# Performance work log

Measured on AMD Instinct MI355X. Metric: run time of the kernel, lower is better.

The kernel has to match this reference:

```python
import jax, jax.numpy as jnp
import numpy as np
from jax import lax

N, E, F, H, B = 16384, 262144, 32, 128, 16
DI, DS, DC, DTR = 256, 16, 4, 8   # Mamba: d_inner=expand*H, d_state, d_conv, dt_rank=ceil(H/16)
NS, NC = 512, 8                   # num_stations, num line colors
EPS = 1e-5


def _forward(node_features, edge_index, batch, W_in, b_in, W_g1, b_g1, W_g2, b_g2,
             W_inproj, conv_w, conv_b, W_xproj, W_dt, b_dt, A_log, D_p, W_out,
             gamma, beta, Wc, bc, Wh, bh, Wt, bt, Wp1, bp1, Wp2, bp2, Wd, bd, Ws, bs):
    def gcn(x, W, b):
        # GCNConv with self-loops and symmetric normalization
        loops = jnp.arange(N)
        s = jnp.concatenate([edge_index[0], loops])
        d = jnp.concatenate([edge_index[1], loops])
        deg = jax.ops.segment_sum(jnp.ones(s.shape[0], x.dtype), d, num_segments=N)
        dinv = jnp.where(deg > 0, lax.rsqrt(deg), 0.0)
        xw = x @ W
        msg = xw[s] * (dinv[s] * dinv[d])[:, None]
        return jax.ops.segment_sum(msg, d, num_segments=N) + b

    h = jax.nn.relu(node_features @ W_in + b_in)
    h = jax.nn.relu(gcn(h, W_g1, b_g1))
    h_gnn = jax.nn.relu(gcn(h, W_g2, b_g2))

    # --- Mamba block over the node sequence (batch dim of 1, seq_len = N) ---
    xz = h_gnn @ W_inproj                      # (N, 2*DI)
    x, z = xz[:, :DI], xz[:, DI:]
    xp = jnp.pad(x, ((DC - 1, 0), (0, 0)))     # causal depthwise conv1d
    xc = conv_b + sum(xp[k:k + N] * conv_w[:, k] for k in range(DC))
    x = jax.nn.silu(xc)
    dbl = x @ W_xproj                          # (N, DTR + 2*DS)
    dt = jax.nn.softplus(dbl[:, :DTR] @ W_dt + b_dt)   # (N, DI)
    Bm = dbl[:, DTR:DTR + DS]                  # (N, DS)
    Cm = dbl[:, DTR + DS:]                     # (N, DS)
    A = -jnp.exp(A_log)                        # (DI, DS)
    dA = jnp.exp(dt[:, :, None] * A[None])     # (N, DI, DS)
    dBx = dt[:, :, None] * Bm[:, None, :] * x[:, :, None]

    def step(hst, t):
        dA_t, dBx_t, C_t = t
        hst = dA_t * hst + dBx_t               # (DI, DS)
        return hst, hst @ C_t                  # (DI,)

    _, ys = lax.scan(step, jnp.zeros((DI, DS), x.dtype), (dA, dBx, Cm))
    y = (ys + D_p * x) * jax.nn.silu(z)
    h_mamba = y @ W_out                        # (N, H)

    # residual + LayerNorm
    hh = h_gnn + h_mamba
    mu = hh.mean(-1, keepdims=True)
    var = ((hh - mu) ** 2).mean(-1, keepdims=True)
    h_final = (hh - mu) * lax.rsqrt(var + EPS) * gamma + beta

    # global_mean_pool per graph
    counts = jax.ops.segment_sum(jnp.ones(N, h_final.dtype), batch, num_segments=B)
    ge = jax.ops.segment_sum(h_final, batch, num_segments=B) / jnp.maximum(counts, 1.0)[:, None]

    # critic + all policy heads, concatenated: [1,4,3,NS,NS,NS,NC]
    return jnp.concatenate([ge @ Wc + bc, ge @ Wh + bh, ge @ Wt + bt,
                            ge @ Wp1 + bp1, ge @ Wp2 + bp2, ge @ Wd + bd,
                            ge @ Ws + bs], axis=-1)


def setup_inputs() -> dict:
    key = jax.random.key(0)
    ks = list(jax.random.split(key, 20))
    p = lambda i, shape, s=0.02: jax.random.normal(ks[i], shape, jnp.float32) * s
    return dict(
        node_features=jax.random.normal(ks[0], (N, F), jnp.float32),
        edge_index=jax.random.randint(ks[1], (2, E), 0, N),
        batch=jnp.sort(jax.random.randint(ks[2], (N,), 0, B)),
        W_in=p(3, (F, H)), b_in=jnp.zeros((H,), jnp.float32),
        W_g1=p(4, (H, H)), b_g1=jnp.zeros((H,), jnp.float32),
        W_g2=p(5, (H, H)), b_g2=jnp.zeros((H,), jnp.float32),
        W_inproj=p(6, (H, 2 * DI)),
        conv_w=p(7, (DI, DC)), conv_b=jnp.zeros((DI,), jnp.float32),
        W_xproj=p(8, (DI, DTR + 2 * DS)),
        W_dt=p(9, (DTR, DI)), b_dt=jnp.full((DI,), -4.0, jnp.float32),
        A_log=jnp.log(jnp.broadcast_to(jnp.arange(1.0, DS + 1.0, dtype=jnp.float32), (DI, DS))),
        D_p=jnp.ones((DI,), jnp.float32),
        W_out=p(10, (DI, H)),
        gamma=jnp.ones((H,), jnp.float32), beta=jnp.zeros((H,), jnp.float32),
        Wc=p(11, (H, 1)), bc=jnp.zeros((1,), jnp.float32),
        Wh=p(12, (H, 4)), bh=jnp.zeros((4,), jnp.float32),
        Wt=p(13, (H, 3)), bt=jnp.zeros((3,), jnp.float32),
        Wp1=p(14, (H, NS)), bp1=jnp.zeros((NS,), jnp.float32),
        Wp2=p(15, (H, NS)), bp2=jnp.zeros((NS,), jnp.float32),
        Wd=p(16, (H, NS)), bd=jnp.zeros((NS,), jnp.float32),
        Ws=p(17, (H, NC)), bs=jnp.zeros((NC,), jnp.float32),
    )


def reference(node_features, edge_index, batch, W_in, b_in, W_g1, b_g1, W_g2, b_g2,
              W_inproj, conv_w, conv_b, W_xproj, W_dt, b_dt, A_log, D_p, W_out,
              gamma, beta, Wc, bc, Wh, bh, Wt, bt, Wp1, bp1, Wp2, bp2, Wd, bd, Ws, bs):
    return _forward(node_features, edge_index, batch, W_in, b_in, W_g1, b_g1, W_g2, b_g2,
                    W_inproj, conv_w, conv_b, W_xproj, W_dt, b_dt, A_log, D_p, W_out,
                    gamma, beta, Wc, bc, Wh, bh, Wt, bt, Wp1, bp1, Wp2, bp2, Wd, bd, Ws, bs)
```

## Files before the change

kernel.cpp:

```cpp
#include <hip/hip_runtime.h>
#include <math.h>

#define NN 16384
#define EE 262144
#define FF 32
#define HH 128
#define BB 16
#define DI 256
#define DS 16
#define DC 4
#define DTR 8
#define OUTW 1552
#define NCH 256
#define CHLEN 64
#define NG 8
#define GL 32

__device__ __forceinline__ float siluf(float v) { return v / (1.f + __expf(-v)); }
__device__ __forceinline__ float softplusf(float v) {
    return fmaxf(v, 0.f) + __logf(1.f + __expf(-fabsf(v)));
}

__global__ void deg_kernel(const int* __restrict__ dst, int* __restrict__ cnt) {
    int e = blockIdx.x * blockDim.x + threadIdx.x;
    if (e < EE) atomicAdd(&cnt[dst[e]], 1);
}

__global__ __launch_bounds__(1024) void prefix_kernel(const int* __restrict__ cnt,
                                                      int* __restrict__ rowptr,
                                                      int* __restrict__ cursor,
                                                      float* __restrict__ dinv) {
    __shared__ int part[1024];
    int tid = threadIdx.x;
    int4 c4[4];
#pragma unroll
    for (int j = 0; j < 4; j++) c4[j] = ((const int4*)cnt)[tid * 4 + j];
    int v[16] = {c4[0].x, c4[0].y, c4[0].z, c4[0].w, c4[1].x, c4[1].y, c4[1].z, c4[1].w,
                 c4[2].x, c4[2].y, c4[2].z, c4[2].w, c4[3].x, c4[3].y, c4[3].z, c4[3].w};
    int s = 0;
#pragma unroll
    for (int j = 0; j < 16; j++) s += v[j];
    part[tid] = s;
    __syncthreads();
    for (int off = 1; off < 1024; off <<= 1) {
        int t = (tid >= off) ? part[tid - off] : 0;
        __syncthreads();
        part[tid] += t;
        __syncthreads();
    }
    int running = part[tid] - s;
    int rp[16];
    float dv[16];
#pragma unroll
    for (int j = 0; j < 16; j++) {
        rp[j] = running;
        running += v[j];
        dv[j] = rsqrtf((float)(v[j] + 1));
    }
#pragma unroll
    for (int j = 0; j < 4; j++) {
        int4 r4; r4.x = rp[j*4]; r4.y = rp[j*4+1]; r4.z = rp[j*4+2]; r4.w = rp[j*4+3];
        ((int4*)rowptr)[tid * 4 + j] = r4;
        ((int4*)cursor)[tid * 4 + j] = r4;
        float4 d4; d4.x = dv[j*4]; d4.y = dv[j*4+1]; d4.z = dv[j*4+2]; d4.w = dv[j*4+3];
        ((float4*)dinv)[tid * 4 + j] = d4;
    }
    if (tid == 1023) rowptr[NN] = part[1023];
}

__global__ void scatter_kernel(const int* __restrict__ src, const int* __restrict__ dst,
                               int* __restrict__ cursor, int* __restrict__ col) {
    int e = blockIdx.x * blockDim.x + threadIdx.x;
    if (e < EE) {
        int d = dst[e];
        int pos = atomicAdd(&cursor[d], 1);
        col[pos] = src[e];
    }
}

__global__ __launch_bounds__(256) void gemm_k(const float* __restrict__ A,
                                              const float* __restrict__ B,
                                              const float* __restrict__ bias,
                                              float* __restrict__ C,
                                              int M, int Nn, int K, int act) {
    __shared__ float As[16][68];
    __shared__ float Bs[16][68];
    int tid = threadIdx.x;
    int m0 = blockIdx.y * 64;
    int n0 = blockIdx.x * 64;
    int ty = tid >> 4, tx = tid & 15;
    float acc[4][4] = {{0.f}};
    for (int k0 = 0; k0 < K; k0 += 16) {
#pragma unroll
        for (int l = 0; l < 4; l++) {
            int idx = tid + l * 256;
            int i = idx >> 4, j = idx & 15;
            As[j][i] = A[(size_t)(m0 + i) * K + k0 + j];
        }
#pragma unroll
        for (int l = 0; l < 4; l++) {
            int idx = tid + l * 256;
            int i = idx >> 6, j = idx & 63;
            int n = n0 + j;
            Bs[i][j] = (n < Nn) ? B[(size_t)(k0 + i) * Nn + n] : 0.f;
        }
        __syncthreads();
#pragma unroll
        for (int kk = 0; kk < 16; kk++) {
            float4 a4 = *(const float4*)&As[kk][ty * 4];
            float4 b4 = *(const float4*)&Bs[kk][tx * 4];
            float av[4] = {a4.x, a4.y, a4.z, a4.w};
            float bv[4] = {b4.x, b4.y, b4.z, b4.w};
#pragma unroll
            for (int r = 0; r < 4; r++)
#pragma unroll
                for (int c = 0; c < 4; c++) acc[r][c] = fmaf(av[r], bv[c], acc[r][c]);
        }
        __syncthreads();
    }
    int nb = n0 + tx * 4;
    if (nb < Nn) {
        float4 bi4 = {0.f, 0.f, 0.f, 0.f};
        if (bias) bi4 = *(const float4*)&bias[nb];
#pragma unroll
        for (int r = 0; r < 4; r++) {
            int m = m0 + ty * 4 + r;
            float4 v;
            v.x = acc[r][0] + bi4.x; v.y = acc[r][1] + bi4.y;
            v.z = acc[r][2] + bi4.z; v.w = acc[r][3] + bi4.w;
            if (act == 1) {
                v.x = fmaxf(v.x, 0.f); v.y = fmaxf(v.y, 0.f);
                v.z = fmaxf(v.z, 0.f); v.w = fmaxf(v.w, 0.f);
            }
            *(float4*)&C[(size_t)m * Nn + nb] = v;
        }
    }
}

__global__ __launch_bounds__(256, 4) void gemm_big(const float* __restrict__ A,
                                                   const float* __restrict__ B,
                                                   float* __restrict__ C,
                                                   int M, int Nn, int K) {
    __shared__ float As[16][132];
    __shared__ float Bs[16][132];
    int tid = threadIdx.x;
    int m0 = blockIdx.y * 128;
    int n0 = blockIdx.x * 128;
    int ty = tid >> 4, tx = tid & 15;
    float acc[8][8] = {{0.f}};
    for (int k0 = 0; k0 < K; k0 += 16) {
        {
            int m = tid >> 1;
            int kc = (tid & 1) * 8;
            const float* ap = &A[(size_t)(m0 + m) * K + k0 + kc];
            float4 a0 = *(const float4*)ap;
            float4 a1 = *(const float4*)(ap + 4);
            As[kc + 0][m] = a0.x; As[kc + 1][m] = a0.y;
            As[kc + 2][m] = a0.z; As[kc + 3][m] = a0.w;
            As[kc + 4][m] = a1.x; As[kc + 5][m] = a1.y;
            As[kc + 6][m] = a1.z; As[kc + 7][m] = a1.w;
        }
        {
            int krow = tid >> 4;
            int c8 = (tid & 15) * 8;
            const float* bp = &B[(size_t)(k0 + krow) * Nn + n0 + c8];
            *(float4*)&Bs[krow][c8] = *(const float4*)bp;
            *(float4*)&Bs[krow][c8 + 4] = *(const float4*)(bp + 4);
        }
        __syncthreads();
#pragma unroll
        for (int kk = 0; kk < 16; kk++) {
            float4 a0 = *(const float4*)&As[kk][ty * 4];
            float4 a1 = *(const float4*)&As[kk][64 + ty * 4];
            float4 b0 = *(const float4*)&Bs[kk][tx * 4];
            float4 b1 = *(const float4*)&Bs[kk][64 + tx * 4];
            float av[8] = {a0.x, a0.y, a0.z, a0.w, a1.x, a1.y, a1.z, a1.w};
            float bv[8] = {b0.x, b0.y, b0.z, b0.w, b1.x, b1.y, b1.z, b1.w};
#pragma unroll
            for (int r = 0; r < 8; r++)
#pragma unroll
                for (int c = 0; c < 8; c++) acc[r][c] = fmaf(av[r], bv[c], acc[r][c]);
        }
        __syncthreads();
    }
#pragma unroll
    for (int r = 0; r < 8; r++) {
        int m = m0 + ((r < 4) ? (ty * 4 + r) : (64 + ty * 4 + r - 4));
        float4 v0, v1;
        v0.x = acc[r][0]; v0.y = acc[r][1]; v0.z = acc[r][2]; v0.w = acc[r][3];
        v1.x = acc[r][4]; v1.y = acc[r][5]; v1.z = acc[r][6]; v1.w = acc[r][7];
        *(float4*)&C[(size_t)m * Nn + n0 + tx * 4] = v0;
        *(float4*)&C[(size_t)m * Nn + n0 + 64 + tx * 4] = v1;
    }
}

__global__ __launch_bounds__(256) void gemm_at_dblt(const float* __restrict__ AT,
                                                    const float* __restrict__ B,
                                                    float* __restrict__ dblt) {
    __shared__ float As[16][68];
    __shared__ float Bs[16][68];
    __shared__ float Ct[64][41];
    int tid = threadIdx.x;
    int m0 = blockIdx.x * 64;
    int ty = tid >> 4, tx = tid & 15;
    float acc[4][4] = {{0.f}};
    for (int k0 = 0; k0 < DI; k0 += 16) {
#pragma unroll
        for (int l = 0; l < 4; l++) {
            int idx = tid + l * 256;
            int kk = idx >> 6, i = idx & 63;
            As[kk][i] = AT[(size_t)(k0 + kk) * NN + m0 + i];
        }
#pragma unroll
        for (int l = 0; l < 4; l++) {
            int idx = tid + l * 256;
            int i = idx >> 6, j = idx & 63;
            Bs[i][j] = (j < 40) ? B[(size_t)(k0 + i) * 40 + j] : 0.f;
        }
        __syncthreads();
#pragma unroll
        for (int kk = 0; kk < 16; kk++) {
            float4 a4 = *(const float4*)&As[kk][ty * 4];
            float4 b4 = *(const float4*)&Bs[kk][tx * 4];
            float av[4] = {a4.x, a4.y, a4.z, a4.w};
            float bv[4] = {b4.x, b4.y, b4.z, b4.w};
#pragma unroll
            for (int r = 0; r < 4; r++)
#pragma unroll
                for (int c = 0; c < 4; c++) acc[r][c] = fmaf(av[r], bv[c], acc[r][c]);
        }
        __syncthreads();
    }
    if (tx * 4 < 40) {
#pragma unroll
        for (int r = 0; r < 4; r++) {
            int m = ty * 4 + r;
            Ct[m][tx * 4 + 0] = acc[r][0];
            Ct[m][tx * 4 + 1] = acc[r][1];
            Ct[m][tx * 4 + 2] = acc[r][2];
            Ct[m][tx * 4 + 3] = acc[r][3];
        }
    }
    __syncthreads();
#pragma unroll
    for (int l = 0; l < 10; l++) {
        int idx = tid + l * 256;
        int n = idx >> 6, m = idx & 63;
        dblt[(size_t)n * NN + m0 + m] = Ct[m][n];
    }
}

__global__ __launch_bounds__(256) void gemm_at_ln(const float* __restrict__ AT,
                                                  const float* __restrict__ B,
                                                  const float* __restrict__ hg,
                                                  const float* __restrict__ gamma,
                                                  const float* __restrict__ beta,
                                                  float* __restrict__ out) {
    __shared__ float As[16][36];
    __shared__ float Bs[16][132];
    int tid = threadIdx.x;
    int m0 = blockIdx.x * 32;
    int ty = tid >> 4, tx = tid & 15;
    float acc[2][8] = {{0.f}};
    for (int k0 = 0; k0 < 256; k0 += 16) {
        {
            int idx = tid * 2;
            int kk = idx >> 5, i = idx & 31;
            As[kk][i] = AT[(size_t)(k0 + kk) * NN + m0 + i];
            As[kk][i + 1] = AT[(size_t)(k0 + kk) * NN + m0 + i + 1];
        }
        {
            int krow = tid >> 4;
            int c8 = (tid & 15) * 8;
            const float* bp = &B[(size_t)(k0 + krow) * HH + c8];
            *(float4*)&Bs[krow][c8] = *(const float4*)bp;
            *(float4*)&Bs[krow][c8 + 4] = *(const float4*)(bp + 4);
        }
        __syncthreads();
#pragma unroll
        for (int kk = 0; kk < 16; kk++) {
            float a0 = As[kk][ty * 2];
            float a1 = As[kk][ty * 2 + 1];
            float4 b0 = *(const float4*)&Bs[kk][tx * 4];
            float4 b1 = *(const float4*)&Bs[kk][64 + tx * 4];
            float bv[8] = {b0.x, b0.y, b0.z, b0.w, b1.x, b1.y, b1.z, b1.w};
#pragma unroll
            for (int c = 0; c < 8; c++) {
                acc[0][c] = fmaf(a0, bv[c], acc[0][c]);
                acc[1][c] = fmaf(a1, bv[c], acc[1][c]);
            }
        }
        __syncthreads();
    }
    float4 g0 = *(const float4*)&gamma[tx * 4];
    float4 g1 = *(const float4*)&gamma[64 + tx * 4];
    float4 be0 = *(const float4*)&beta[tx * 4];
    float4 be1 = *(const float4*)&beta[64 + tx * 4];
    float gv[8] = {g0.x, g0.y, g0.z, g0.w, g1.x, g1.y, g1.z, g1.w};
    float bv[8] = {be0.x, be0.y, be0.z, be0.w, be1.x, be1.y, be1.z, be1.w};
#pragma unroll
    for (int r = 0; r < 2; r++) {
        int m = m0 + ty * 2 + r;
        float4 h0 = *(const float4*)&hg[(size_t)m * HH + tx * 4];
        float4 h1 = *(const float4*)&hg[(size_t)m * HH + 64 + tx * 4];
        float v[8] = {acc[r][0] + h0.x, acc[r][1] + h0.y, acc[r][2] + h0.z, acc[r][3] + h0.w,
                      acc[r][4] + h1.x, acc[r][5] + h1.y, acc[r][6] + h1.z, acc[r][7] + h1.w};
        float sum = 0.f;
#pragma unroll
        for (int c = 0; c < 8; c++) sum += v[c];
        sum += __shfl_xor(sum, 1); sum += __shfl_xor(sum, 2);
        sum += __shfl_xor(sum, 4); sum += __shfl_xor(sum, 8);
        float mu = sum * (1.f / 128.f);
        float vs = 0.f;
#pragma unroll
        for (int c = 0; c < 8; c++) { float dd = v[c] - mu; vs += dd * dd; }
        vs += __shfl_xor(vs, 1); vs += __shfl_xor(vs, 2);
        vs += __shfl_xor(vs, 4); vs += __shfl_xor(vs, 8);
        float inv = rsqrtf(vs * (1.f / 128.f) + 1e-5f);
        float4 o0, o1;
        o0.x = (v[0] - mu) * inv * gv[0] + bv[0];
        o0.y = (v[1] - mu) * inv * gv[1] + bv[1];
        o0.z = (v[2] - mu) * inv * gv[2] + bv[2];
        o0.w = (v[3] - mu) * inv * gv[3] + bv[3];
        o1.x = (v[4] - mu) * inv * gv[4] + bv[4];
        o1.y = (v[5] - mu) * inv * gv[5] + bv[5];
        o1.z = (v[6] - mu) * inv * gv[6] + bv[6];
        o1.w = (v[7] - mu) * inv * gv[7] + bv[7];
        *(float4*)&out[(size_t)m * HH + tx * 4] = o0;
        *(float4*)&out[(size_t)m * HH + 64 + tx * 4] = o1;
    }
}

__global__ __launch_bounds__(256) void gcn_gather4(const float* __restrict__ xw,
                                                   const int* __restrict__ rowptr,
                                                   const int* __restrict__ col,
                                                   const float* __restrict__ dinv,
                                                   const float* __restrict__ b,
                                                   float* __restrict__ out) {
    int tid = threadIdx.x;
    int sub = tid & 31;
    int n = blockIdx.x * 8 + (tid >> 5);
    float dn = dinv[n];
    const float4* xw4 = (const float4*)xw;
    float4 a = xw4[(size_t)n * 32 + sub];
    float ws = dn * dn;
    float4 acc;
    acc.x = a.x * ws; acc.y = a.y * ws; acc.z = a.z * ws; acc.w = a.w * ws;
    int beg = rowptr[n], end = rowptr[n + 1];
    int e = beg;
    for (; e + 4 <= end; e += 4) {
        int s0 = col[e], s1 = col[e + 1], s2 = col[e + 2], s3 = col[e + 3];
        float w0 = dinv[s0] * dn, w1 = dinv[s1] * dn;
        float w2 = dinv[s2] * dn, w3 = dinv[s3] * dn;
        float4 v0 = xw4[(size_t)s0 * 32 + sub];
        float4 v1 = xw4[(size_t)s1 * 32 + sub];
        float4 v2 = xw4[(size_t)s2 * 32 + sub];
        float4 v3 = xw4[(size_t)s3 * 32 + sub];
        acc.x = fmaf(v0.x, w0, acc.x); acc.y = fmaf(v0.y, w0, acc.y);
        acc.z = fmaf(v0.z, w0, acc.z); acc.w = fmaf(v0.w, w0, acc.w);
        acc.x = fmaf(v1.x, w1, acc.x); acc.y = fmaf(v1.y, w1, acc.y);
        acc.z = fmaf(v1.z, w1, acc.z); acc.w = fmaf(v1.w, w1, acc.w);
        acc.x = fmaf(v2.x, w2, acc.x); acc.y = fmaf(v2.y, w2, acc.y);
        acc.z = fmaf(v2.z, w2, acc.z); acc.w = fmaf(v2.w, w2, acc.w);
        acc.x = fmaf(v3.x, w3, acc.x); acc.y = fmaf(v3.y, w3, acc.y);
        acc.z = fmaf(v3.z, w3, acc.z); acc.w = fmaf(v3.w, w3, acc.w);
    }
    for (; e < end; e++) {
        int s0 = col[e];
        float w0 = dinv[s0] * dn;
        float4 v0 = xw4[(size_t)s0 * 32 + sub];
        acc.x = fmaf(v0.x, w0, acc.x); acc.y = fmaf(v0.y, w0, acc.y);
        acc.z = fmaf(v0.z, w0, acc.z); acc.w = fmaf(v0.w, w0, acc.w);
    }
    float4 b4 = ((const float4*)b)[sub];
    acc.x = fmaxf(acc.x + b4.x, 0.f);
    acc.y = fmaxf(acc.y + b4.y, 0.f);
    acc.z = fmaxf(acc.z + b4.z, 0.f);
    acc.w = fmaxf(acc.w + b4.w, 0.f);
    ((float4*)out)[(size_t)n * 32 + sub] = acc;
}

__global__ __launch_bounds__(256) void conv_silu_t(const float* __restrict__ xz,
                                                   const float* __restrict__ cw,
                                                   const float* __restrict__ cb,
                                                   float* __restrict__ xst,
                                                   float* __restrict__ szt) {
    __shared__ float tile[67][65];
    int tid = threadIdx.x;
    int t0 = blockIdx.x * 64;
    int c0 = blockIdx.y * 64;
#pragma unroll
    for (int l = 0; l < 17; l++) {
        int idx = tid + l * 256;
        if (idx < 67 * 64) {
            int r = idx >> 6, c = idx & 63;
            int gt = t0 - 3 + r;
            tile[r][c] = (gt >= 0) ? xz[(size_t)gt * 512 + c0 + c] : 0.f;
        }
    }
    __syncthreads();
    int tl = tid & 63;
    int d0 = tid >> 6;
    if (c0 < 256) {
#pragma unroll
        for (int l = 0; l < 16; l++) {
            int dl = d0 + l * 4;
            int dg = c0 + dl;
            float acc = cb[dg];
#pragma unroll
            for (int k = 0; k < DC; k++)
                acc = fmaf(tile[tl + k][dl], cw[dg * DC + k], acc);
            xst[dg * NN + t0 + tl] = siluf(acc);
        }
    } else {
#pragma unroll
        for (int l = 0; l < 16; l++) {
            int dl = d0 + l * 4;
            int dg = c0 - 256 + dl;
            szt[dg * NN + t0 + tl] = siluf(tile[tl + 3][dl]);
        }
    }
}

__global__ __launch_bounds__(256, 6) void scan_phase1(const float* __restrict__ xst,
                                                      const float* __restrict__ dblt,
                                                      const float* __restrict__ A_log,
                                                      const float* __restrict__ W_dt,
                                                      const float* __restrict__ b_dt,
                                                      float* __restrict__ chkP,
                                                      float* __restrict__ chkH) {
    __shared__ float Td[32][68];
    __shared__ float Tx[32][68];
    __shared__ float Bs[16][68];
    __shared__ float D8[8][68];
    int tid = threadIdx.x;
    int wave = tid >> 6, lane = tid & 63;
    int sg = lane & 7, dl = lane >> 3;
    int dblk = blockIdx.x, chunk = blockIdx.y;
    int t0 = chunk * CHLEN;
    int dloc = wave * 8 + dl;
    int d = dblk * 32 + dloc;
    int s0 = 2 * sg;
#pragma unroll
    for (int p = 0; p < 2; p++) {
        int linear = tid + p * 256;
        int row = linear >> 4, c4 = (linear & 15) * 4;
        *(float4*)&Tx[row][c4] = *(const float4*)&xst[(size_t)(dblk * 32 + row) * NN + t0 + c4];
    }
    if (tid < 128) {
        int r = tid >> 4, c4 = (tid & 15) * 4;
        *(float4*)&D8[r][c4] = *(const float4*)&dblt[(size_t)r * NN + t0 + c4];
    }
    {
        int s = tid >> 4, c4 = (tid & 15) * 4;
        *(float4*)&Bs[s][c4] = *(const float4*)&dblt[(size_t)(8 + s) * NN + t0 + c4];
    }
    float A0 = -expf(A_log[d * DS + s0]);
    float A1 = -expf(A_log[d * DS + s0 + 1]);
    __syncthreads();
    {
        int row = tid >> 3;
        int tb = (tid & 7) * 8;
        int dd = dblk * 32 + row;
        float bd = b_dt[dd];
        float wv[8];
#pragma unroll
        for (int j = 0; j < 8; j++) wv[j] = W_dt[j * DI + dd];
#pragma unroll
        for (int j = 0; j < 8; j++) {
            int t = tb + j;
            float acc = bd;
#pragma unroll
            for (int k = 0; k < 8; k++) acc = fmaf(D8[k][t], wv[k], acc);
            Td[row][t] = softplusf(acc);
        }
    }
    __syncthreads();
    float h0 = 0.f, h1 = 0.f, P0 = 1.f, P1 = 1.f;
    for (int i = 0; i < CHLEN; i += 4) {
        float4 d4 = *(const float4*)&Td[dloc][i];
        float4 x4 = *(const float4*)&Tx[dloc][i];
        float4 b04 = *(const float4*)&Bs[s0][i];
        float4 b14 = *(const float4*)&Bs[s0 + 1][i];
#define P1S(U) { float dtv = d4.U; float a0 = __expf(dtv * A0); float a1 = __expf(dtv * A1); \
        float dx = dtv * x4.U; h0 = fmaf(a0, h0, dx * b04.U); h1 = fmaf(a1, h1, dx * b14.U); \
        P0 *= a0; P1 *= a1; }
        P1S(x) P1S(y) P1S(z) P1S(w)
#undef P1S
    }
    int idx = chunk * 4096 + d * DS + s0;
    float2 vP; vP.x = P0; vP.y = P1;
    float2 vH; vH.x = h0; vH.y = h1;
    *(float2*)(chkP + idx) = vP;
    *(float2*)(chkH + idx) = vH;
}

__global__ void scan_phase2a(const float* __restrict__ chkP, const float* __restrict__ chkH,
                             float* __restrict__ gp, float* __restrict__ gh) {
    int g = blockIdx.x * blockDim.x + threadIdx.x;
    int idx = g & 4095;
    int grp = g >> 12;
    int c0 = grp * GL;
    float P = 1.f, H = 0.f;
    for (int j = 0; j < GL; j += 4) {
        float p[4], q[4];
#pragma unroll
        for (int jj = 0; jj < 4; jj++) {
            p[jj] = chkP[(c0 + j + jj) * 4096 + idx];
            q[jj] = chkH[(c0 + j + jj) * 4096 + idx];
        }
#pragma unroll
        for (int jj = 0; jj < 4; jj++) {
            H = fmaf(p[jj], H, q[jj]);
            P *= p[jj];
        }
    }
    gp[grp * 4096 + idx] = P;
    gh[grp * 4096 + idx] = H;
}

__global__ void scan_phase2c(const float* __restrict__ chkP, const float* __restrict__ chkH,
                             const float* __restrict__ gp, const float* __restrict__ gh,
                             float* __restrict__ init) {
    int g = blockIdx.x * blockDim.x + threadIdx.x;
    int idx = g & 4095;
    int grp = g >> 12;
    int c0 = grp * GL;
    float h = 0.f;
    for (int gg = 0; gg < grp; gg++)
        h = fmaf(gp[gg * 4096 + idx], h, gh[gg * 4096 + idx]);
    for (int j = 0; j < GL; j += 4) {
        float p[4], q[4];
#pragma unroll
        for (int jj = 0; jj < 4; jj++) {
            p[jj] = chkP[(c0 + j + jj) * 4096 + idx];
            q[jj] = chkH[(c0 + j + jj) * 4096 + idx];
        }
#pragma unroll
        for (int jj = 0; jj < 4; jj++) {
            init[(c0 + j + jj) * 4096 + idx] = h;
            h = fmaf(p[jj], h, q[jj]);
        }
    }
}

__global__ __launch_bounds__(256, 5) void scan_phase3(const float* __restrict__ xst,
                                                      const float* __restrict__ dblt,
                                                      const float* __restrict__ A_log,
                                                      const float* __restrict__ W_dt,
                                                      const float* __restrict__ b_dt,
                                                      const float* __restrict__ init,
                                                      const float* __restrict__ D_p,
                                                      const float* __restrict__ szt,
                                                      float* __restrict__ yt) {
    __shared__ float Td[32][68];
    __shared__ float Tx[32][68];
    __shared__ float Bs[16][68];
    __shared__ float Cs[16][68];
    __shared__ float D8[8][68];
    int tid = threadIdx.x;
    int wave = tid >> 6, lane = tid & 63;
    int sg = lane & 7, dl = lane >> 3;
    int dblk = blockIdx.x, chunk = blockIdx.y;
    int t0 = chunk * CHLEN;
    int dloc = wave * 8 + dl;
    int d = dblk * 32 + dloc;
    int s0 = 2 * sg;
#pragma unroll
    for (int p = 0; p < 2; p++) {
        int linear = tid + p * 256;
        int row = linear >> 4, c4 = (linear & 15) * 4;
        *(float4*)&Tx[row][c4] = *(const float4*)&xst[(size_t)(dblk * 32 + row) * NN + t0 + c4];
    }
    if (tid < 128) {
        int r = tid >> 4, c4 = (tid & 15) * 4;
        *(float4*)&D8[r][c4] = *(const float4*)&dblt[(size_t)r * NN + t0 + c4];
    }
    {
        int s = tid >> 4, c4 = (tid & 15) * 4;
        *(float4*)&Bs[s][c4] = *(const float4*)&dblt[(size_t)(8 + s) * NN + t0 + c4];
        *(float4*)&Cs[s][c4] = *(const float4*)&dblt[(size_t)(24 + s) * NN + t0 + c4];
    }
    float A0 = -expf(A_log[d * DS + s0]);
    float A1 = -expf(A_log[d * DS + s0 + 1]);
    float Dd = D_p[d];
    float2 ini = *(const float2*)(init + chunk * 4096 + d * DS + s0);
    float h0 = ini.x, h1 = ini.y;
    __syncthreads();
    {
        int row = tid >> 3;
        int tb = (tid & 7) * 8;
        int dd = dblk * 32 + row;
        float bd = b_dt[dd];
        float wv[8];
#pragma unroll
        for (int j = 0; j < 8; j++) wv[j] = W_dt[j * DI + dd];
#pragma unroll
        for (int j = 0; j < 8; j++) {
            int t = tb + j;
            float acc = bd;
#pragma unroll
            for (int k = 0; k < 8; k++) acc = fmaf(D8[k][t], wv[k], acc);
            Td[row][t] = softplusf(acc);
        }
    }
    __syncthreads();
    for (int i = 0; i < CHLEN; i += 4) {
        float4 d4 = *(const float4*)&Td[dloc][i];
        float4 x4 = *(const float4*)&Tx[dloc][i];
        float4 b04 = *(const float4*)&Bs[s0][i];
        float4 b14 = *(const float4*)&Bs[s0 + 1][i];
        float4 c04 = *(const float4*)&Cs[s0][i];
        float4 c14 = *(const float4*)&Cs[s0 + 1][i];
        float4 yv;
#define P3S(U) { float dtv = d4.U; float a0 = __expf(dtv * A0); float a1 = __expf(dtv * A1); \
        float dx = dtv * x4.U; h0 = fmaf(a0, h0, dx * b04.U); h1 = fmaf(a1, h1, dx * b14.U); \
        float c = fmaf(h1, c14.U, h0 * c04.U); \
        c += __shfl_xor(c, 1); c += __shfl_xor(c, 2); c += __shfl_xor(c, 4); \
        yv.U = c + Dd * x4.U; }
        P3S(x) P3S(y) P3S(z) P3S(w)
#undef P3S
        if (sg == 0) *(float4*)&Td[dloc][i] = yv;
    }
#pragma unroll
    for (int r = 0; r < 8; r++) {
        int row = wave * 8 + r;
        float sz = szt[(size_t)(dblk * 32 + row) * NN + t0 + lane];
        yt[(size_t)(dblk * 32 + row) * NN + t0 + lane] = Td[row][lane] * sz;
    }
}

__global__ void pool_kernel(const float* __restrict__ hf, const int* __restrict__ batch,
                            float* __restrict__ ge, int* __restrict__ counts) {
    int f = threadIdx.x;
    int r0 = blockIdx.x * 128;
    int gcur = batch[r0];
    float acc = 0.f;
    int cnt = 0;
    for (int i = 0; i < 128; i += 4) {
        int r = r0 + i;
        int g0 = batch[r], g3 = batch[r + 3];
        float v0 = hf[(size_t)r * HH + f];
        float v1 = hf[(size_t)(r + 1) * HH + f];
        float v2 = hf[(size_t)(r + 2) * HH + f];
        float v3 = hf[(size_t)(r + 3) * HH + f];
        if (g0 == gcur && g3 == gcur) {
            acc += (v0 + v1) + (v2 + v3);
            cnt += 4;
        } else {
            int gs[4] = {g0, batch[r + 1], batch[r + 2], g3};
            float vs[4] = {v0, v1, v2, v3};
#pragma unroll
            for (int k = 0; k < 4; k++) {
                if (gs[k] != gcur) {
                    atomicAdd(&ge[gcur * HH + f], acc);
                    if (f == 0) atomicAdd(&counts[gcur], cnt);
                    acc = 0.f; cnt = 0; gcur = gs[k];
                }
                acc += vs[k];
                cnt++;
            }
        }
    }
    atomicAdd(&ge[gcur * HH + f], acc);
    if (f == 0) atomicAdd(&counts[gcur], cnt);
}

__global__ void heads_kernel(const float* __restrict__ ge, const int* __restrict__ counts,
                             const float* Wc, const float* bc, const float* Wh, const float* bh,
                             const float* Wt, const float* bt, const float* Wp1, const float* bp1,
                             const float* Wp2, const float* bp2, const float* Wd, const float* bd,
                             const float* Ws, const float* bs, float* __restrict__ out) {
    int col = blockIdx.x * blockDim.x + threadIdx.x;
    int b = blockIdx.y;
    if (col >= OUTW) return;
    const float* W; const float* bi; int lc, w;
    if (col < 1)         { W = Wc;  bi = bc;  lc = col;        w = 1; }
    else if (col < 5)    { W = Wh;  bi = bh;  lc = col - 1;    w = 4; }
    else if (col < 8)    { W = Wt;  bi = bt;  lc = col - 5;    w = 3; }
    else if (col < 520)  { W = Wp1; bi = bp1; lc = col - 8;    w = 512; }
    else if (col < 1032) { W = Wp2; bi = bp2; lc = col - 520;  w = 512; }
    else if (col < 1544) { W = Wd;  bi = bd;  lc = col - 1032; w = 512; }
    else                 { W = Ws;  bi = bs;  lc = col - 1544; w = 8; }
    float scale = 1.f / fmaxf((float)counts[b], 1.f);
    float dot = 0.f;
#pragma unroll 8
    for (int f = 0; f < HH; f++) dot = fmaf(ge[b * HH + f], W[f * w + lc], dot);
    out[(size_t)b * OUTW + col] = bi[lc] + scale * dot;
}

extern "C" void kernel_launch(void* const* d_in, const int* in_sizes, int n_in,
                              void* d_out, int out_size, void* d_ws, size_t ws_size,
                              hipStream_t stream) {
    const float* nf      = (const float*)d_in[0];
    const int*   ei      = (const int*)d_in[1];
    const int*   batch   = (const int*)d_in[2];
    const float* W_in    = (const float*)d_in[3];
    const float* b_in    = (const float*)d_in[4];
    const float* W_g1    = (const float*)d_in[5];
    const float* b_g1    = (const float*)d_in[6];
    const float* W_g2    = (const float*)d_in[7];
    const float* b_g2    = (const float*)d_in[8];
    const float* W_inproj= (const float*)d_in[9];
    const float* conv_w  = (const float*)d_in[10];
    const float* conv_b  = (const float*)d_in[11];
    const float* W_xproj = (const float*)d_in[12];
    const float* W_dt    = (const float*)d_in[13];
    const float* b_dt    = (const float*)d_in[14];
    const float* A_log   = (const float*)d_in[15];
    const float* D_p     = (const float*)d_in[16];
    const float* W_out   = (const float*)d_in[17];
    const float* gamma   = (const float*)d_in[18];
    const float* beta    = (const float*)d_in[19];
    const float* Wc = (const float*)d_in[20]; const float* bc = (const float*)d_in[21];
    const float* Wh = (const float*)d_in[22]; const float* bh = (const float*)d_in[23];
    const float* Wt = (const float*)d_in[24]; const float* bt = (const float*)d_in[25];
    const float* Wp1= (const float*)d_in[26]; const float* bp1= (const float*)d_in[27];
    const float* Wp2= (const float*)d_in[28]; const float* bp2= (const float*)d_in[29];
    const float* Wd = (const float*)d_in[30]; const float* bd = (const float*)d_in[31];
    const float* Ws = (const float*)d_in[32]; const float* bs = (const float*)d_in[33];

    const int* e_src = ei;
    const int* e_dst = ei + EE;

    float* w = (float*)d_ws;
    size_t o = 0;
    float* F0   = w + o; o += (size_t)NN * HH;
    float* F1   = w + o; o += (size_t)NN * HH;
    float* F2   = w + o; o += (size_t)NN * HH;
    float* XZ   = w + o; o += (size_t)NN * 512;
    float* YT   = XZ;
    float* XST  = w + o; o += (size_t)NN * DI;
    float* SZT  = w + o; o += (size_t)NN * DI;
    float* DBL  = w + o; o += (size_t)NN * 40;
    float* DBLT = w + o; o += (size_t)NN * 40;
    float* GE   = w + o; o += BB * HH;
    float* DINV = w + o; o += NN;
    int* ip = (int*)(w + o);
    int* CNT    = ip; ip += NN;
    int* ROWPTR = ip; ip += NN + 1;
    int* CURSOR = ip; ip += NN;
    int* COL    = ip; ip += EE;
    int* COUNTS = ip; ip += BB;

    float* CHP  = F0;
    float* CHH  = F0 + (size_t)NCH * 4096;
    float* INI  = F1;
    float* GP   = DBL;
    float* GH   = DBL + NG * 4096;

    hipMemsetAsync(CNT, 0, NN * sizeof(int), stream);
    hipMemsetAsync(GE, 0, BB * HH * sizeof(float), stream);
    hipMemsetAsync(COUNTS, 0, BB * sizeof(int), stream);

    deg_kernel<<<EE / 256, 256, 0, stream>>>(e_dst, CNT);
    prefix_kernel<<<1, 1024, 0, stream>>>(CNT, ROWPTR, CURSOR, DINV);
    scatter_kernel<<<EE / 256, 256, 0, stream>>>(e_src, e_dst, CURSOR, COL);

    gemm_k<<<dim3(2, NN / 64), 256, 0, stream>>>(nf, W_in, b_in, F0, NN, HH, FF, 1);
    gemm_k<<<dim3(2, NN / 64), 256, 0, stream>>>(F0, W_g1, nullptr, F1, NN, HH, HH, 0);
    gcn_gather4<<<NN / 8, 256, 0, stream>>>(F1, ROWPTR, COL, DINV, b_g1, F0);
    gemm_k<<<dim3(2, NN / 64), 256, 0, stream>>>(F0, W_g2, nullptr, F1, NN, HH, HH, 0);
    gcn_gather4<<<NN / 8, 256, 0, stream>>>(F1, ROWPTR, COL, DINV, b_g2, F2);

    gemm_big<<<dim3(4, NN / 128), 256, 0, stream>>>(F2, W_inproj, XZ, NN, 512, HH);
    conv_silu_t<<<dim3(NN / 64, 8), 256, 0, stream>>>(XZ, conv_w, conv_b, XST, SZT);
    gemm_at_dblt<<<NN / 64, 256, 0, stream>>>(XST, W_xproj, DBLT);

    scan_phase1<<<dim3(8, NCH), 256, 0, stream>>>(XST, DBLT, A_log, W_dt, b_dt, CHP, CHH);
    scan_phase2a<<<(4096 * NG) / 256, 256, 0, stream>>>(CHP, CHH, GP, GH);
    scan_phase2c<<<(4096 * NG) / 256, 256, 0, stream>>>(CHP, CHH, GP, GH, INI);
    scan_phase3<<<dim3(8, NCH), 256, 0, stream>>>(XST, DBLT, A_log, W_dt, b_dt, INI, D_p, SZT, YT);

    gemm_at_ln<<<NN / 32, 256, 0, stream>>>(YT, W_out, F2, gamma, beta, F0);

    pool_kernel<<<NN / 128, HH, 0, stream>>>(F0, batch, GE, COUNTS);

    heads_kernel<<<dim3((OUTW + 127) / 128, BB), 128, 0, stream>>>(
        GE, COUNTS, Wc, bc, Wh, bh, Wt, bt, Wp1, bp1, Wp2, bp2, Wd, bd, Ws, bs, (float*)d_out);
}
```

Measured before the change: 412.8 us.

## Merge scan phase-2 kernels, fuse memsets into zero kernel, trim scan_phase3 LDS

```diff
diff --git a/kernel.cpp b/kernel.cpp
--- a/kernel.cpp
+++ b/kernel.cpp
@@ -13,12 +13,18 @@
 #define OUTW 1552
 #define NCH 256
 #define CHLEN 64
-#define NG 8
-#define GL 32
 
 __device__ __forceinline__ float siluf(float v) { return v / (1.f + __expf(-v)); }
 __device__ __forceinline__ float softplusf(float v) {
     return fmaxf(v, 0.f) + __logf(1.f + __expf(-fabsf(v)));
+}
+
+__global__ void zero_kernel(int* __restrict__ cnt, float* __restrict__ ge,
+                            int* __restrict__ counts) {
+    int idx = blockIdx.x * blockDim.x + threadIdx.x;
+    if (idx < NN) cnt[idx] = 0;
+    if (idx < BB * HH) ge[idx] = 0.f;
+    if (idx < BB) counts[idx] = 0;
 }
 
 __global__ void deg_kernel(const int* __restrict__ dst, int* __restrict__ cnt) {
@@ -495,56 +501,26 @@
     *(float2*)(chkH + idx) = vH;
 }
 
-__global__ void scan_phase2a(const float* __restrict__ chkP, const float* __restrict__ chkH,
-                             float* __restrict__ gp, float* __restrict__ gh) {
-    int g = blockIdx.x * blockDim.x + threadIdx.x;
-    int idx = g & 4095;
-    int grp = g >> 12;
-    int c0 = grp * GL;
-    float P = 1.f, H = 0.f;
-    for (int j = 0; j < GL; j += 4) {
-        float p[4], q[4];
-#pragma unroll
-        for (int jj = 0; jj < 4; jj++) {
-            p[jj] = chkP[(c0 + j + jj) * 4096 + idx];
-            q[jj] = chkH[(c0 + j + jj) * 4096 + idx];
-        }
-#pragma unroll
-        for (int jj = 0; jj < 4; jj++) {
-            H = fmaf(p[jj], H, q[jj]);
-            P *= p[jj];
-        }
-    }
-    gp[grp * 4096 + idx] = P;
-    gh[grp * 4096 + idx] = H;
-}
-
-__global__ void scan_phase2c(const float* __restrict__ chkP, const float* __restrict__ chkH,
-                             const float* __restrict__ gp, const float* __restrict__ gh,
-                             float* __restrict__ init) {
-    int g = blockIdx.x * blockDim.x + threadIdx.x;
-    int idx = g & 4095;
-    int grp = g >> 12;
-    int c0 = grp * GL;
+__global__ void scan_phase2(const float* __restrict__ chkP, const float* __restrict__ chkH,
+                            float* __restrict__ init) {
+    int idx = blockIdx.x * blockDim.x + threadIdx.x;
     float h = 0.f;
-    for (int gg = 0; gg < grp; gg++)
-        h = fmaf(gp[gg * 4096 + idx], h, gh[gg * 4096 + idx]);
-    for (int j = 0; j < GL; j += 4) {
-        float p[4], q[4];
-#pragma unroll
-        for (int jj = 0; jj < 4; jj++) {
-            p[jj] = chkP[(c0 + j + jj) * 4096 + idx];
-            q[jj] = chkH[(c0 + j + jj) * 4096 + idx];
-        }
-#pragma unroll
-        for (int jj = 0; jj < 4; jj++) {
-            init[(c0 + j + jj) * 4096 + idx] = h;
-            h = fmaf(p[jj], h, q[jj]);
-        }
-    }
-}
-
-__global__ __launch_bounds__(256, 5) void scan_phase3(const float* __restrict__ xst,
+    for (int c0 = 0; c0 < NCH; c0 += 8) {
+        float p[8], q[8];
+#pragma unroll
+        for (int j = 0; j < 8; j++) {
+            p[j] = chkP[(c0 + j) * 4096 + idx];
+            q[j] = chkH[(c0 + j) * 4096 + idx];
+        }
+#pragma unroll
+        for (int j = 0; j < 8; j++) {
+            init[(c0 + j) * 4096 + idx] = h;
+            h = fmaf(p[j], h, q[j]);
+        }
+    }
+}
+
+__global__ __launch_bounds__(256, 6) void scan_phase3(const float* __restrict__ xst,
                                                       const float* __restrict__ dblt,
                                                       const float* __restrict__ A_log,
                                                       const float* __restrict__ W_dt,
@@ -556,8 +532,7 @@
     __shared__ float Td[32][68];
     __shared__ float Tx[32][68];
     __shared__ float Bs[16][68];
-    __shared__ float Cs[16][68];
-    __shared__ float D8[8][68];
+    __shared__ float CsD8[16][68];
     int tid = threadIdx.x;
     int wave = tid >> 6, lane = tid & 63;
     int sg = lane & 7, dl = lane >> 3;
@@ -574,12 +549,11 @@
     }
     if (tid < 128) {
         int r = tid >> 4, c4 = (tid & 15) * 4;
-        *(float4*)&D8[r][c4] = *(const float4*)&dblt[(size_t)r * NN + t0 + c4];
+        *(float4*)&CsD8[r][c4] = *(const float4*)&dblt[(size_t)r * NN + t0 + c4];
     }
     {
         int s = tid >> 4, c4 = (tid & 15) * 4;
         *(float4*)&Bs[s][c4] = *(const float4*)&dblt[(size_t)(8 + s) * NN + t0 + c4];
-        *(float4*)&Cs[s][c4] = *(const float4*)&dblt[(size_t)(24 + s) * NN + t0 + c4];
     }
     float A0 = -expf(A_log[d * DS + s0]);
     float A1 = -expf(A_log[d * DS + s0 + 1]);
@@ -600,9 +574,14 @@
             int t = tb + j;
             float acc = bd;
 #pragma unroll
-            for (int k = 0; k < 8; k++) acc = fmaf(D8[k][t], wv[k], acc);
+            for (int k = 0; k < 8; k++) acc = fmaf(CsD8[k][t], wv[k], acc);
             Td[row][t] = softplusf(acc);
         }
+    }
+    __syncthreads();
+    {
+        int s = tid >> 4, c4 = (tid & 15) * 4;
+        *(float4*)&CsD8[s][c4] = *(const float4*)&dblt[(size_t)(24 + s) * NN + t0 + c4];
     }
     __syncthreads();
     for (int i = 0; i < CHLEN; i += 4) {
@@ -610,8 +589,8 @@
         float4 x4 = *(const float4*)&Tx[dloc][i];
         float4 b04 = *(const float4*)&Bs[s0][i];
         float4 b14 = *(const float4*)&Bs[s0 + 1][i];
-        float4 c04 = *(const float4*)&Cs[s0][i];
-        float4 c14 = *(const float4*)&Cs[s0 + 1][i];
+        float4 c04 = *(const float4*)&CsD8[s0][i];
+        float4 c14 = *(const float4*)&CsD8[s0 + 1][i];
         float4 yv;
 #define P3S(U) { float dtv = d4.U; float a0 = __expf(dtv * A0); float a1 = __expf(dtv * A1); \
         float dx = dtv * x4.U; h0 = fmaf(a0, h0, dx * b04.U); h1 = fmaf(a1, h1, dx * b14.U); \
@@ -633,11 +612,11 @@
 __global__ void pool_kernel(const float* __restrict__ hf, const int* __restrict__ batch,
                             float* __restrict__ ge, int* __restrict__ counts) {
     int f = threadIdx.x;
-    int r0 = blockIdx.x * 128;
+    int r0 = blockIdx.x * 64;
     int gcur = batch[r0];
     float acc = 0.f;
     int cnt = 0;
-    for (int i = 0; i < 128; i += 4) {
+    for (int i = 0; i < 64; i += 4) {
         int r = r0 + i;
         int g0 = batch[r], g3 = batch[r + 3];
         float v0 = hf[(size_t)r * HH + f];
@@ -732,7 +711,6 @@
     float* YT   = XZ;
     float* XST  = w + o; o += (size_t)NN * DI;
     float* SZT  = w + o; o += (size_t)NN * DI;
-    float* DBL  = w + o; o += (size_t)NN * 40;
     float* DBLT = w + o; o += (size_t)NN * 40;
     float* GE   = w + o; o += BB * HH;
     float* DINV = w + o; o += NN;
@@ -746,12 +724,8 @@
     float* CHP  = F0;
     float* CHH  = F0 + (size_t)NCH * 4096;
     float* INI  = F1;
-    float* GP   = DBL;
-    float* GH   = DBL + NG * 4096;
-
-    hipMemsetAsync(CNT, 0, NN * sizeof(int), stream);
-    hipMemsetAsync(GE, 0, BB * HH * sizeof(float), stream);
-    hipMemsetAsync(COUNTS, 0, BB * sizeof(int), stream);
+
+    zero_kernel<<<(NN + 255) / 256, 256, 0, stream>>>(CNT, GE, COUNTS);
 
     deg_kernel<<<EE / 256, 256, 0, stream>>>(e_dst, CNT);
     prefix_kernel<<<1, 1024, 0, stream>>>(CNT, ROWPTR, CURSOR, DINV);
@@ -768,13 +742,12 @@
     gemm_at_dblt<<<NN / 64, 256, 0, stream>>>(XST, W_xproj, DBLT);
 
     scan_phase1<<<dim3(8, NCH), 256, 0, stream>>>(XST, DBLT, A_log, W_dt, b_dt, CHP, CHH);
-    scan_phase2a<<<(4096 * NG) / 256, 256, 0, stream>>>(CHP, CHH, GP, GH);
-    scan_phase2c<<<(4096 * NG) / 256, 256, 0, stream>>>(CHP, CHH, GP, GH, INI);
+    scan_phase2<<<16, 256, 0, stream>>>(CHP, CHH, INI);
     scan_phase3<<<dim3(8, NCH), 256, 0, stream>>>(XST, DBLT, A_log, W_dt, b_dt, INI, D_p, SZT, YT);
 
     gemm_at_ln<<<NN / 32, 256, 0, stream>>>(YT, W_out, F2, gamma, beta, F0);
 
-    pool_kernel<<<NN / 128, HH, 0, stream>>>(F0, batch, GE, COUNTS);
+    pool_kernel<<<NN / 64, HH, 0, stream>>>(F0, batch, GE, COUNTS);
 
     heads_kernel<<<dim3((OUTW + 127) / 128, BB), 128, 0, stream>>>(
         GE, COUNTS, Wc, bc, Wh, bh, Wt, bt, Wp1, bp1, Wp2, bp2, Wd, bd, Ws, bs, (float*)d_out);
```

Result: no change. 407.9 us (-1.2%).
